# Kernel tuning notes

Hardware: AMD Instinct MI355X
Metric: run time of the kernel (lower is better)

## Reference

```python
import jax, jax.numpy as jnp
import numpy as np

D = 1024  # model_dim; d_ff == model_dim in this module
EPS = 1e-6

def setup_inputs() -> dict:
    key = jax.random.key(0)
    ks = jax.random.split(key, 8)
    s = 1.0 / np.sqrt(D)
    sg = 1.0 / np.sqrt(2 * D)
    return {
        "x": jax.random.normal(ks[0], (8, 2048, D), dtype=jnp.float32),
        "w1": jax.random.uniform(ks[1], (D, D), jnp.float32, -s, s),
        "b1": jnp.zeros((D,), jnp.float32),
        "w2": jax.random.uniform(ks[2], (D, D), jnp.float32, -s, s),
        "b2": jnp.zeros((D,), jnp.float32),
        "ln_g": jnp.ones((D,), jnp.float32),
        "ln_b": jnp.zeros((D,), jnp.float32),
        "wg": jax.random.uniform(ks[3], (2 * D, 2 * D), jnp.float32, -sg, sg),
        "bg": jnp.zeros((2 * D,), jnp.float32),
    }

def _layernorm(x, g, b):
    mu = jnp.mean(x, axis=-1, keepdims=True)
    var = jnp.mean(jnp.square(x - mu), axis=-1, keepdims=True)
    return (x - mu) * jax.lax.rsqrt(var + EPS) * g + b

def reference(x, w1, b1, w2, b2, ln_g, ln_b, wg, bg):
    B, S, d = x.shape
    # cumulative average: tril-normalized mask matmul == prefix-sum / position
    denom = jnp.arange(1, S + 1, dtype=x.dtype)[:, None]  # [S,1]
    avg = jnp.cumsum(x, axis=1) / denom                    # [B,S,D]
    # PositionwiseFeedForward (dropout is identity at inference)
    inter = jax.nn.relu(_layernorm(avg, ln_g, ln_b) @ w1 + b1)
    avg_out = inter @ w2 + b2 + avg
    # gating
    gates = jnp.concatenate([x, avg_out], axis=-1) @ wg + bg  # [B,S,2D]
    in_g, fg_g = jnp.split(gates, 2, axis=-1)
    gated = jax.nn.sigmoid(in_g) * x + jax.nn.sigmoid(fg_g) * avg_out
    return gated, avg_out
```

## Files before the change

### kernel.cpp

```cpp
#include <hip/hip_runtime.h>

typedef unsigned short u16;
typedef __attribute__((ext_vector_type(8))) short short8;
typedef __attribute__((ext_vector_type(8))) unsigned short ushort8;
typedef __attribute__((ext_vector_type(4))) float f32x4;
typedef __attribute__((ext_vector_type(4))) unsigned short u16x4;

#define DEV static __device__ __forceinline__

DEV u16 f2bf(float f){
    unsigned u = __float_as_uint(f);
    u += 0x7fffu + ((u >> 16) & 1u);
    return (u16)(u >> 16);
}
DEV float bf2f(u16 h){ return __uint_as_float(((unsigned)h) << 16); }
DEV float sigm(float v){ return 1.f / (1.f + __expf(-v)); }

DEV f32x4 MF(short8 a, short8 b, f32x4 c){
    return __builtin_amdgcn_mfma_f32_16x16x32_bf16(a, b, c, 0, 0, 0);
}
DEV void gload16(const void* g, u16* l){
    __builtin_amdgcn_global_load_lds(
        (const __attribute__((address_space(1))) void*)g,
        (__attribute__((address_space(3))) void*)l, 16, 0, 0);
}
DEV void stage_half(const char* gp, size_t K2, u16* dst){
    gload16(gp, dst);
    gload16(gp + (K2 << 3), dst + 512);
}

#define SBAR()   asm volatile("s_barrier" ::: "memory")
#define WVM(n)   asm volatile("s_waitcnt vmcnt(" #n ")" ::: "memory")
#define WLG(n)   asm volatile("s_waitcnt lgkmcnt(" #n ")" ::: "memory")
#define SCB()    __builtin_amdgcn_sched_barrier(0)

constexpr int Bn = 8, Sn = 2048, Dn = 1024;
constexpr int CH = 128, NC = Sn / CH;
constexpr size_t NTOK = (size_t)Bn * Sn;

__global__ __launch_bounds__(256) void k_wcvt(const float* __restrict__ w,
                                              u16* __restrict__ wt,
                                              int Kd, int Nd)
{
    __shared__ float tile[32][33];
    int nbn = Nd / 32;
    int bk = blockIdx.x / nbn, bn = blockIdx.x % nbn;
    int lx = threadIdx.x & 31, ly = threadIdx.x >> 5;
    #pragma unroll
    for (int i = 0; i < 32; i += 8)
        tile[ly + i][lx] = w[(size_t)(bk * 32 + ly + i) * Nd + bn * 32 + lx];
    __syncthreads();
    #pragma unroll
    for (int i = 0; i < 32; i += 8)
        wt[(size_t)(bn * 32 + ly + i) * Kd + bk * 32 + lx] = f2bf(tile[lx][ly + i]);
}

__global__ __launch_bounds__(256) void k_psum(const float* __restrict__ x,
                                              float* __restrict__ part)
{
    int bx = blockIdx.x;
    int dblk = bx & 3; bx >>= 2;
    int c = bx & (NC - 1), b = bx >> 4;
    int d = dblk * 256 + threadIdx.x;
    const float* px = x + ((size_t)b * Sn + (size_t)c * CH) * Dn + d;
    float s = 0.f;
    #pragma unroll 4
    for (int i = 0; i < CH; i++) s += px[(size_t)i * Dn];
    part[((size_t)b * NC + c) * Dn + d] = s;
}

__global__ __launch_bounds__(256) void k_pscan(float* part)
{
    int g = blockIdx.x * 256 + threadIdx.x;
    int b = g >> 10, d = g & 1023;
    float run = 0.f;
    #pragma unroll
    for (int c = 0; c < NC; c++){
        size_t idx = ((size_t)b * NC + c) * Dn + d;
        float v = part[idx]; part[idx] = run; run += v;
    }
}

__global__ __launch_bounds__(256) void k_avg(const float* __restrict__ x,
                                             const float* __restrict__ part,
                                             u16* __restrict__ avg,
                                             u16* __restrict__ cat)
{
    int bx = blockIdx.x;
    int dblk = bx & 3; bx >>= 2;
    int c = bx & (NC - 1), b = bx >> 4;
    int d = dblk * 256 + threadIdx.x;
    const float* px = x   + ((size_t)b * Sn + (size_t)c * CH) * Dn + d;
    u16*         pa = avg + ((size_t)b * Sn + (size_t)c * CH) * Dn + d;
    u16*         pc = cat + ((size_t)b * Sn + (size_t)c * CH) * 2048 + d;
    float run = part[((size_t)b * NC + c) * Dn + d];
    for (int i = 0; i < CH; i++){
        float v = px[(size_t)i * Dn];
        run += v;
        int s = c * CH + i;
        pa[(size_t)i * Dn] = f2bf(run / (float)(s + 1));
        pc[(size_t)i * 2048] = f2bf(v);
    }
}

__global__ __launch_bounds__(256) void k_ln(const u16* __restrict__ avg,
                                            const float* __restrict__ g,
                                            const float* __restrict__ bta,
                                            u16* __restrict__ out)
{
    size_t row = blockIdx.x;
    int t = threadIdx.x;
    u16x4 hv = ((const u16x4*)(avg + row * Dn))[t];
    float4 v = { bf2f(hv[0]), bf2f(hv[1]), bf2f(hv[2]), bf2f(hv[3]) };
    float s = v.x + v.y + v.z + v.w;
    float q = v.x * v.x + v.y * v.y + v.z * v.z + v.w * v.w;
    #pragma unroll
    for (int o = 32; o > 0; o >>= 1){
        s += __shfl_down(s, o, 64);
        q += __shfl_down(q, o, 64);
    }
    __shared__ float rs[4], rq[4];
    __shared__ float smu, srstd;
    int wid = t >> 6, lane = t & 63;
    if (lane == 0){ rs[wid] = s; rq[wid] = q; }
    __syncthreads();
    if (t == 0){
        float S = rs[0] + rs[1] + rs[2] + rs[3];
        float Q = rq[0] + rq[1] + rq[2] + rq[3];
        float mu = S * (1.f / Dn);
        float var = Q * (1.f / Dn) - mu * mu;
        smu = mu; srstd = rsqrtf(var + 1e-6f);
    }
    __syncthreads();
    float mu = smu, rstd = srstd;
    int d0 = t * 4;
    float4 gg = ((const float4*)g)[t];
    float4 bb = ((const float4*)bta)[t];
    u16x4 o;
    o[0] = f2bf((v.x - mu) * rstd * gg.x + bb.x);
    o[1] = f2bf((v.y - mu) * rstd * gg.y + bb.y);
    o[2] = f2bf((v.z - mu) * rstd * gg.z + bb.z);
    o[3] = f2bf((v.w - mu) * rstd * gg.w + bb.w);
    *(u16x4*)(out + row * Dn + d0) = o;
}

template<int EPI>
__global__ __launch_bounds__(512, 2)
void k_gemm(const u16* __restrict__ A, const u16* __restrict__ Bt,
            const float* __restrict__ bias,
            float* __restrict__ of, u16* __restrict__ ob,
            const u16* __restrict__ resid,
            int M, int N, int K)
{
    __shared__ u16 smem[2][2][2][8192];

    int nbn = (EPI == 3) ? 8 : (N >> 8);
    int nwg = (M >> 8) * nbn;
    int bid = blockIdx.x;
    int swz = (bid & 7) * (nwg >> 3) + (bid >> 3);
    int bm = swz / nbn, bn = swz - bm * nbn;
    int m0 = bm << 8;
    int n0 = (EPI == 3) ? (bn << 7) : (bn << 8);

    int tid  = threadIdx.x;
    int wid  = tid >> 6, lane = tid & 63;
    int wm   = wid >> 2, wn = wid & 3;
    int fr   = lane & 15, q = lane >> 4;

    int srow = (wid << 4) + (lane >> 3);
    int cb   = ((lane & 7) << 4) ^ (((lane >> 3) & 7) << 4);
    size_t K2 = (size_t)K * 2;
    int b1base = (EPI == 3) ? (1024 + n0) : (n0 + 128);
    const char* gA0 = (const char*)A  + (size_t)(m0 + srow) * K2 + cb;
    const char* gA1 = (const char*)A  + (size_t)(m0 + 128 + srow) * K2 + cb;
    const char* gB0 = (const char*)Bt + (size_t)(n0 + srow) * K2 + cb;
    const char* gB1 = (const char*)Bt + (size_t)(b1base + srow) * K2 + cb;
    int w16 = wid << 10;

    int xorE = (lane & 7) << 3;
    int cbE0 = ((q << 3) ^ xorE);
    int cbE1 = cbE0 ^ 32;
    int aOff = (wm * 64 + fr) * 64;
    int bOff = (wn * 32 + fr) * 64;

    f32x4 acc[8][4] = {};
    short8 a0f[4][2], a1f[4][2], b0f[2][2], b1f[2][2];
    int NT = K >> 6;

#define ST_A0(t) stage_half(gA0 + (size_t)(t) * 128, K2, &smem[(t)&1][0][0][w16])
#define ST_A1(t) stage_half(gA1 + (size_t)(t) * 128, K2, &smem[(t)&1][0][1][w16])
#define ST_B0(t) stage_half(gB0 + (size_t)(t) * 128, K2, &smem[(t)&1][1][0][w16])
#define ST_B1(t) stage_half(gB1 + (size_t)(t) * 128, K2, &smem[(t)&1][1][1][w16])
#define RD_A(Fr, t, half) { const u16* _p = &smem[(t)&1][0][half][0];           \
    _Pragma("unroll") for (int i = 0; i < 4; i++){                              \
        Fr[i][0] = *(const short8*)&_p[aOff + i * 1024 + cbE0];                 \
        Fr[i][1] = *(const short8*)&_p[aOff + i * 1024 + cbE1]; } }
#define RD_B(Fr, t, half) { const u16* _p = &smem[(t)&1][1][half][0];           \
    _Pragma("unroll") for (int i = 0; i < 2; i++){                              \
        Fr[i][0] = *(const short8*)&_p[bOff + i * 1024 + cbE0];                 \
        Fr[i][1] = *(const short8*)&_p[bOff + i * 1024 + cbE1]; } }
#define MMQ(Af, Bf, mo, no)                                                     \
    __builtin_amdgcn_s_setprio(1);                                              \
    _Pragma("unroll") for (int k = 0; k < 2; k++)                               \
        _Pragma("unroll") for (int mi = 0; mi < 4; mi++)                        \
            _Pragma("unroll") for (int ni = 0; ni < 2; ni++)                    \
                acc[mi+(mo)][ni+(no)] = MF(Af[mi][k], Bf[ni][k],                \
                                           acc[mi+(mo)][ni+(no)]);              \
    __builtin_amdgcn_s_setprio(0);

    ST_A0(0); ST_B0(0); ST_A1(0); ST_B1(0);

    for (int t = 0; t + 1 < NT; ++t){
        WVM(4); SBAR();
        ST_A0(t + 1);
        RD_A(a0f, t, 0);
        RD_B(b0f, t, 0);
        WLG(0); SCB();
        MMQ(a0f, b0f, 0, 0);
        WVM(4); SBAR();
        ST_B0(t + 1);
        RD_A(a1f, t, 1);
        WLG(0); SCB();
        MMQ(a1f, b0f, 4, 0);
        WVM(4); SBAR();
        ST_A1(t + 1);
        RD_B(b1f, t, 1);
        WLG(0); SCB();
        MMQ(a1f, b1f, 4, 2);
        ST_B1(t + 1);
        MMQ(a0f, b1f, 0, 2);
    }
    {
        int t = NT - 1;
        WVM(4); SBAR();
        RD_A(a0f, t, 0);
        RD_B(b0f, t, 0);
        WLG(0); SCB();
        MMQ(a0f, b0f, 0, 0);
        WVM(2); SBAR();
        RD_A(a1f, t, 1);
        WLG(0); SCB();
        MMQ(a1f, b0f, 4, 0);
        WVM(0); SBAR();
        RD_B(b1f, t, 1);
        WLG(0); SCB();
        MMQ(a1f, b1f, 4, 2);
        MMQ(a0f, b1f, 0, 2);
    }

    int col = lane & 15, rb = q * 4;

    if constexpr (EPI == 3){
        u16* s_in = &smem[0][0][0][0];
        u16* s_fg = s_in + 32768;
        float bi[2], bf_[2];
        #pragma unroll
        for (int ni = 0; ni < 2; ni++){
            bi[ni]  = bias[n0 + wn * 32 + ni * 16 + col];
            bf_[ni] = bias[1024 + n0 + wn * 32 + ni * 16 + col];
        }
        SBAR();
        #pragma unroll
        for (int mi = 0; mi < 8; mi++){
            int lrow = ((mi & 4) << 5) + wm * 64 + ((mi & 3) << 4) + rb;
            #pragma unroll
            for (int ni = 0; ni < 2; ni++){
                int c  = wn * 32 + ni * 16 + col;
                int cp = c ^ (q << 4);
                #pragma unroll
                for (int r = 0; r < 4; r++){
                    int row = lrow + r;
                    s_in[row * 128 + cp] = f2bf(sigm(acc[mi][ni][r] + bi[ni]));
                    s_fg[row * 128 + cp] = f2bf(sigm(acc[mi][ni + 2][r] + bf_[ni]));
                }
            }
        }
        WLG(0); SBAR();
        int rbase = wid * 32;
        #pragma unroll
        for (int rg = 0; rg < 8; rg++){
            int b4  = rbase + rg * 4;
            int row = b4 + (lane >> 4);
            int sw  = ((b4 >> 2) & 3) << 4;
            int c0  = (lane & 15) * 8;
            int cp  = c0 ^ sw;
            ushort8 iv = *(const ushort8*)&s_in[row * 128 + cp];
            ushort8 fv = *(const ushort8*)&s_fg[row * 128 + cp];
            size_t ga = (size_t)(m0 + row) * 2048 + n0 + c0;
            ushort8 xv = *(const ushort8*)&A[ga];
            ushort8 av = *(const ushort8*)&A[ga + 1024];
            size_t gb = (size_t)(m0 + row) * Dn + n0 + c0;
            float4 o0, o1;
            o0.x = bf2f(iv[0]) * bf2f(xv[0]) + bf2f(fv[0]) * bf2f(av[0]);
            o0.y = bf2f(iv[1]) * bf2f(xv[1]) + bf2f(fv[1]) * bf2f(av[1]);
            o0.z = bf2f(iv[2]) * bf2f(xv[2]) + bf2f(fv[2]) * bf2f(av[2]);
            o0.w = bf2f(iv[3]) * bf2f(xv[3]) + bf2f(fv[3]) * bf2f(av[3]);
            o1.x = bf2f(iv[4]) * bf2f(xv[4]) + bf2f(fv[4]) * bf2f(av[4]);
            o1.y = bf2f(iv[5]) * bf2f(xv[5]) + bf2f(fv[5]) * bf2f(av[5]);
            o1.z = bf2f(iv[6]) * bf2f(xv[6]) + bf2f(fv[6]) * bf2f(av[6]);
            o1.w = bf2f(iv[7]) * bf2f(xv[7]) + bf2f(fv[7]) * bf2f(av[7]);
            *(float4*)&of[gb] = o0;
            *(float4*)&of[gb + 4] = o1;
        }
        return;
    }

    #pragma unroll
    for (int mi = 0; mi < 8; mi++){
        int lrow = m0 + ((mi & 4) << 5) + wm * 64 + ((mi & 3) << 4) + rb;
        #pragma unroll
        for (int ni = 0; ni < 4; ni++){
            int gn = n0 + ((ni & 2) << 6) + wn * 32 + ((ni & 1) << 4) + col;
            float bv = bias[gn];
            #pragma unroll
            for (int r = 0; r < 4; r++){
                int gm = lrow + r;
                float v = acc[mi][ni][r] + bv;
                if constexpr (EPI == 1){
                    ob[(size_t)gm * N + gn] = f2bf(fmaxf(v, 0.f));
                } else {
                    v += bf2f(resid[(size_t)gm * N + gn]);
                    of[(size_t)gm * N + gn] = v;
                    ob[(size_t)gm * 2 * N + N + gn] = f2bf(v);
                }
            }
        }
    }
}

extern "C" void kernel_launch(void* const* d_in, const int* in_sizes, int n_in,
                              void* d_out, int out_size, void* d_ws, size_t ws_size,
                              hipStream_t stream)
{
    const float* x   = (const float*)d_in[0];
    const float* w1  = (const float*)d_in[1];
    const float* b1  = (const float*)d_in[2];
    const float* w2  = (const float*)d_in[3];
    const float* b2  = (const float*)d_in[4];
    const float* lng = (const float*)d_in[5];
    const float* lnb = (const float*)d_in[6];
    const float* wg  = (const float*)d_in[7];
    const float* bg  = (const float*)d_in[8];

    float* gated   = (float*)d_out;
    float* avg_out = (float*)d_out + NTOK * Dn;

    char* ws = (char*)d_ws;
    u16*   w1t   = (u16*)  (ws + (0ull   << 20));
    u16*   w2t   = (u16*)  (ws + (2ull   << 20));
    u16*   wgt   = (u16*)  (ws + (4ull   << 20));
    float* part  = (float*)(ws + (12ull  << 20));
    u16*   avg   = (u16*)  (ws + (16ull  << 20));
    u16*   ln    = (u16*)  (ws + (80ull  << 20));
    u16*   inter = (u16*)  (ws + (112ull << 20));
    u16*   cat   = (u16*)  (ws + (144ull << 20));

    k_wcvt<<<dim3(32 * 32), 256, 0, stream>>>(w1, w1t, Dn, Dn);
    k_wcvt<<<dim3(32 * 32), 256, 0, stream>>>(w2, w2t, Dn, Dn);
    k_wcvt<<<dim3(64 * 64), 256, 0, stream>>>(wg, wgt, 2 * Dn, 2 * Dn);

    k_psum <<<dim3(Bn * NC * 4), 256, 0, stream>>>(x, part);
    k_pscan<<<dim3(Bn * Dn / 256), 256, 0, stream>>>(part);
    k_avg  <<<dim3(Bn * NC * 4), 256, 0, stream>>>(x, part, avg, cat);

    k_ln<<<dim3((int)NTOK), 256, 0, stream>>>(avg, lng, lnb, ln);

    k_gemm<1><<<dim3((int)(NTOK / 256) * (Dn / 256)), 512, 0, stream>>>(
        ln, w1t, b1, nullptr, inter, nullptr, (int)NTOK, Dn, Dn);
    k_gemm<2><<<dim3((int)(NTOK / 256) * (Dn / 256)), 512, 0, stream>>>(
        inter, w2t, b2, avg_out, cat, avg, (int)NTOK, Dn, Dn);

    k_gemm<3><<<dim3((int)(NTOK / 256) * 8), 512, 0, stream>>>(
        cat, wgt, bg, gated, nullptr, nullptr, (int)NTOK, 2 * Dn, 2 * Dn);
}
```

Measured before the change: 304.0 us.

## Rewrite GEMM main loop with BK=32 single-stage pipeline and templated M-tile

Replaces the quarter-staged 256x256, BK=64 GEMM loop with a simpler double-buffered loop that uses BK=32 and stages whole A/B tiles each iteration. The M-tile is now a template parameter: the first two GEMMs use 128-row tiles, doubling the grid, and the gate GEMM keeps 256 rows. The gate epilogue is reorganised so each warp covers input and forget halves in separate columns and writes through LDS in two passes. Intent is to raise occupancy and parallelism and simplify scheduling. The cost is more barriers per unit of K and the loss of the fine-grained load/compute interleave.

```diff
diff --git a/kernel.cpp b/kernel.cpp
--- a/kernel.cpp
+++ b/kernel.cpp
@@ -23,10 +23,6 @@
     __builtin_amdgcn_global_load_lds(
         (const __attribute__((address_space(1))) void*)g,
         (__attribute__((address_space(3))) void*)l, 16, 0, 0);
-}
-DEV void stage_half(const char* gp, size_t K2, u16* dst){
-    gload16(gp, dst);
-    gload16(gp + (K2 << 3), dst + 512);
 }
 
 #define SBAR()   asm volatile("s_barrier" ::: "memory")
@@ -144,7 +140,7 @@
     *(u16x4*)(out + row * Dn + d0) = o;
 }
 
-template<int EPI>
+template<int EPI, int BM>
 __global__ __launch_bounds__(512, 2)
 void k_gemm(const u16* __restrict__ A, const u16* __restrict__ Bt,
             const float* __restrict__ bias,
@@ -152,14 +148,17 @@
             const u16* __restrict__ resid,
             int M, int N, int K)
 {
-    __shared__ u16 smem[2][2][2][8192];
+    constexpr int MFR  = BM / 32;
+    constexpr int AL   = BM / 128;
+    constexpr int HALF = (BM + 256) * 32;
+    __shared__ u16 smem[2 * HALF];
 
     int nbn = (EPI == 3) ? 8 : (N >> 8);
-    int nwg = (M >> 8) * nbn;
+    int nwg = (M / BM) * nbn;
     int bid = blockIdx.x;
     int swz = (bid & 7) * (nwg >> 3) + (bid >> 3);
     int bm = swz / nbn, bn = swz - bm * nbn;
-    int m0 = bm << 8;
+    int m0 = bm * BM;
     int n0 = (EPI == 3) ? (bn << 7) : (bn << 8);
 
     int tid  = threadIdx.x;
@@ -167,155 +166,139 @@
     int wm   = wid >> 2, wn = wid & 3;
     int fr   = lane & 15, q = lane >> 4;
 
-    int srow = (wid << 4) + (lane >> 3);
-    int cb   = ((lane & 7) << 4) ^ (((lane >> 3) & 7) << 4);
+    int l4 = (lane & 3) << 4;
+    int lr = lane >> 2;
     size_t K2 = (size_t)K * 2;
-    int b1base = (EPI == 3) ? (1024 + n0) : (n0 + 128);
-    const char* gA0 = (const char*)A  + (size_t)(m0 + srow) * K2 + cb;
-    const char* gA1 = (const char*)A  + (size_t)(m0 + 128 + srow) * K2 + cb;
-    const char* gB0 = (const char*)Bt + (size_t)(n0 + srow) * K2 + cb;
-    const char* gB1 = (const char*)Bt + (size_t)(b1base + srow) * K2 + cb;
-    int w16 = wid << 10;
-
-    int xorE = (lane & 7) << 3;
-    int cbE0 = ((q << 3) ^ xorE);
-    int cbE1 = cbE0 ^ 32;
-    int aOff = (wm * 64 + fr) * 64;
-    int bOff = (wn * 32 + fr) * 64;
-
-    f32x4 acc[8][4] = {};
-    short8 a0f[4][2], a1f[4][2], b0f[2][2], b1f[2][2];
-    int NT = K >> 6;
-
-#define ST_A0(t) stage_half(gA0 + (size_t)(t) * 128, K2, &smem[(t)&1][0][0][w16])
-#define ST_A1(t) stage_half(gA1 + (size_t)(t) * 128, K2, &smem[(t)&1][0][1][w16])
-#define ST_B0(t) stage_half(gB0 + (size_t)(t) * 128, K2, &smem[(t)&1][1][0][w16])
-#define ST_B1(t) stage_half(gB1 + (size_t)(t) * 128, K2, &smem[(t)&1][1][1][w16])
-#define RD_A(Fr, t, half) { const u16* _p = &smem[(t)&1][0][half][0];           \
-    _Pragma("unroll") for (int i = 0; i < 4; i++){                              \
-        Fr[i][0] = *(const short8*)&_p[aOff + i * 1024 + cbE0];                 \
-        Fr[i][1] = *(const short8*)&_p[aOff + i * 1024 + cbE1]; } }
-#define RD_B(Fr, t, half) { const u16* _p = &smem[(t)&1][1][half][0];           \
-    _Pragma("unroll") for (int i = 0; i < 2; i++){                              \
-        Fr[i][0] = *(const short8*)&_p[bOff + i * 1024 + cbE0];                 \
-        Fr[i][1] = *(const short8*)&_p[bOff + i * 1024 + cbE1]; } }
-#define MMQ(Af, Bf, mo, no)                                                     \
-    __builtin_amdgcn_s_setprio(1);                                              \
-    _Pragma("unroll") for (int k = 0; k < 2; k++)                               \
-        _Pragma("unroll") for (int mi = 0; mi < 4; mi++)                        \
-            _Pragma("unroll") for (int ni = 0; ni < 2; ni++)                    \
-                acc[mi+(mo)][ni+(no)] = MF(Af[mi][k], Bf[ni][k],                \
-                                           acc[mi+(mo)][ni+(no)]);              \
-    __builtin_amdgcn_s_setprio(0);
-
-    ST_A0(0); ST_B0(0); ST_A1(0); ST_B1(0);
-
-    for (int t = 0; t + 1 < NT; ++t){
-        WVM(4); SBAR();
-        ST_A0(t + 1);
-        RD_A(a0f, t, 0);
-        RD_B(b0f, t, 0);
+    const char* gA = (const char*)A + (size_t)(m0 + wid * (BM / 8) + lr) * K2 + l4;
+    int brow = n0 + wid * 32 + lr;
+    if (EPI == 3 && wid >= 4) brow += 896;
+    const char* gB = (const char*)Bt + (size_t)brow * K2 + l4;
+    int aDst = (wid * (BM / 8)) * 32;
+    int bDst = BM * 32 + (wid * 32) * 32;
+
+    int aOff = (wm * (BM / 2) + fr) * 32 + (q << 3);
+    int bOff = BM * 32 + (wn * 64 + fr) * 32 + (q << 3);
+
+    f32x4 acc[MFR][4] = {};
+    short8 af[MFR], bf[4];
+    int NT = K >> 5;
+
+#define STAGE(t) {                                                          \
+    u16* _bp = smem + (((t) & 1) ? HALF : 0);                               \
+    _Pragma("unroll")                                                       \
+    for (int j = 0; j < AL; j++)                                            \
+        gload16(gA + (size_t)(t) * 64 + (size_t)j * 16 * K2,                \
+                _bp + aDst + j * 512);                                      \
+    _Pragma("unroll")                                                       \
+    for (int j = 0; j < 2; j++)                                             \
+        gload16(gB + (size_t)(t) * 64 + (size_t)j * 16 * K2,                \
+                _bp + bDst + j * 512);                                      \
+}
+
+    STAGE(0);
+    for (int t = 0; t < NT; ++t){
+        WVM(0); SBAR();
+        if (t + 1 < NT) STAGE(t + 1);
+        const u16* cp = smem + ((t & 1) ? HALF : 0);
+        #pragma unroll
+        for (int ni = 0; ni < 4; ni++)
+            bf[ni] = *(const short8*)&cp[bOff + ni * 512];
+        #pragma unroll
+        for (int mi = 0; mi < 4; mi++)
+            af[mi] = *(const short8*)&cp[aOff + mi * 512];
         WLG(0); SCB();
-        MMQ(a0f, b0f, 0, 0);
-        WVM(4); SBAR();
-        ST_B0(t + 1);
-        RD_A(a1f, t, 1);
-        WLG(0); SCB();
-        MMQ(a1f, b0f, 4, 0);
-        WVM(4); SBAR();
-        ST_A1(t + 1);
-        RD_B(b1f, t, 1);
-        WLG(0); SCB();
-        MMQ(a1f, b1f, 4, 2);
-        ST_B1(t + 1);
-        MMQ(a0f, b1f, 0, 2);
-    }
-    {
-        int t = NT - 1;
-        WVM(4); SBAR();
-        RD_A(a0f, t, 0);
-        RD_B(b0f, t, 0);
-        WLG(0); SCB();
-        MMQ(a0f, b0f, 0, 0);
-        WVM(2); SBAR();
-        RD_A(a1f, t, 1);
-        WLG(0); SCB();
-        MMQ(a1f, b0f, 4, 0);
-        WVM(0); SBAR();
-        RD_B(b1f, t, 1);
-        WLG(0); SCB();
-        MMQ(a1f, b1f, 4, 2);
-        MMQ(a0f, b1f, 0, 2);
+        __builtin_amdgcn_s_setprio(1);
+        #pragma unroll
+        for (int mi = 0; mi < 4; mi++)
+            #pragma unroll
+            for (int ni = 0; ni < 4; ni++)
+                acc[mi][ni] = MF(af[mi], bf[ni], acc[mi][ni]);
+        __builtin_amdgcn_s_setprio(0);
+        if constexpr (MFR == 8){
+            #pragma unroll
+            for (int mi = 0; mi < 4; mi++)
+                af[mi + 4] = *(const short8*)&cp[aOff + (mi + 4) * 512];
+            WLG(0); SCB();
+            __builtin_amdgcn_s_setprio(1);
+            #pragma unroll
+            for (int mi = 0; mi < 4; mi++)
+                #pragma unroll
+                for (int ni = 0; ni < 4; ni++)
+                    acc[mi + 4][ni] = MF(af[mi + 4], bf[ni], acc[mi + 4][ni]);
+            __builtin_amdgcn_s_setprio(0);
+        }
     }
 
     int col = lane & 15, rb = q * 4;
 
     if constexpr (EPI == 3){
-        u16* s_in = &smem[0][0][0][0];
-        u16* s_fg = s_in + 32768;
-        float bi[2], bf_[2];
-        #pragma unroll
-        for (int ni = 0; ni < 2; ni++){
-            bi[ni]  = bias[n0 + wn * 32 + ni * 16 + col];
-            bf_[ni] = bias[1024 + n0 + wn * 32 + ni * 16 + col];
+        u16* s_in = smem;
+        u16* s_fg = smem + 16384;
+        float bv[4];
+        #pragma unroll
+        for (int ni = 0; ni < 4; ni++){
+            int c = (wn & 1) * 64 + ni * 16 + col;
+            bv[ni] = bias[((wn < 2) ? n0 : 1024 + n0) + c];
         }
-        SBAR();
-        #pragma unroll
-        for (int mi = 0; mi < 8; mi++){
-            int lrow = ((mi & 4) << 5) + wm * 64 + ((mi & 3) << 4) + rb;
-            #pragma unroll
-            for (int ni = 0; ni < 2; ni++){
-                int c  = wn * 32 + ni * 16 + col;
-                int cp = c ^ (q << 4);
+        #pragma unroll
+        for (int p = 0; p < 2; p++){
+            SBAR();
+            if (wm == p){
                 #pragma unroll
-                for (int r = 0; r < 4; r++){
-                    int row = lrow + r;
-                    s_in[row * 128 + cp] = f2bf(sigm(acc[mi][ni][r] + bi[ni]));
-                    s_fg[row * 128 + cp] = f2bf(sigm(acc[mi][ni + 2][r] + bf_[ni]));
+                for (int mi = 0; mi < 8; mi++){
+                    #pragma unroll
+                    for (int ni = 0; ni < 4; ni++){
+                        int c  = (wn & 1) * 64 + ni * 16 + col;
+                        u16* dst = (wn < 2) ? s_in : s_fg;
+                        #pragma unroll
+                        for (int r = 0; r < 4; r++){
+                            int row = mi * 16 + rb + r;
+                            int cpx = c ^ (((row >> 2) & 3) << 4);
+                            dst[row * 128 + cpx] =
+                                f2bf(sigm(acc[mi][ni][r] + bv[ni]));
+                        }
+                    }
                 }
             }
-        }
-        WLG(0); SBAR();
-        int rbase = wid * 32;
-        #pragma unroll
-        for (int rg = 0; rg < 8; rg++){
-            int b4  = rbase + rg * 4;
-            int row = b4 + (lane >> 4);
-            int sw  = ((b4 >> 2) & 3) << 4;
-            int c0  = (lane & 15) * 8;
-            int cp  = c0 ^ sw;
-            ushort8 iv = *(const ushort8*)&s_in[row * 128 + cp];
-            ushort8 fv = *(const ushort8*)&s_fg[row * 128 + cp];
-            size_t ga = (size_t)(m0 + row) * 2048 + n0 + c0;
-            ushort8 xv = *(const ushort8*)&A[ga];
-            ushort8 av = *(const ushort8*)&A[ga + 1024];
-            size_t gb = (size_t)(m0 + row) * Dn + n0 + c0;
-            float4 o0, o1;
-            o0.x = bf2f(iv[0]) * bf2f(xv[0]) + bf2f(fv[0]) * bf2f(av[0]);
-            o0.y = bf2f(iv[1]) * bf2f(xv[1]) + bf2f(fv[1]) * bf2f(av[1]);
-            o0.z = bf2f(iv[2]) * bf2f(xv[2]) + bf2f(fv[2]) * bf2f(av[2]);
-            o0.w = bf2f(iv[3]) * bf2f(xv[3]) + bf2f(fv[3]) * bf2f(av[3]);
-            o1.x = bf2f(iv[4]) * bf2f(xv[4]) + bf2f(fv[4]) * bf2f(av[4]);
-            o1.y = bf2f(iv[5]) * bf2f(xv[5]) + bf2f(fv[5]) * bf2f(av[5]);
-            o1.z = bf2f(iv[6]) * bf2f(xv[6]) + bf2f(fv[6]) * bf2f(av[6]);
-            o1.w = bf2f(iv[7]) * bf2f(xv[7]) + bf2f(fv[7]) * bf2f(av[7]);
-            *(float4*)&of[gb] = o0;
-            *(float4*)&of[gb + 4] = o1;
+            WLG(0); SBAR();
+            #pragma unroll
+            for (int rg = 0; rg < 4; rg++){
+                int row_l = wid * 16 + rg * 4 + q;
+                int grow  = m0 + p * 128 + row_l;
+                int c0 = fr * 8;
+                int cpx = c0 ^ (((row_l >> 2) & 3) << 4);
+                ushort8 iv = *(const ushort8*)&s_in[row_l * 128 + cpx];
+                ushort8 fv = *(const ushort8*)&s_fg[row_l * 128 + cpx];
+                size_t ga = (size_t)grow * 2048 + n0 + c0;
+                ushort8 xv = *(const ushort8*)&A[ga];
+                ushort8 av = *(const ushort8*)&A[ga + 1024];
+                size_t gb = (size_t)grow * Dn + n0 + c0;
+                float4 o0, o1;
+                o0.x = bf2f(iv[0]) * bf2f(xv[0]) + bf2f(fv[0]) * bf2f(av[0]);
+                o0.y = bf2f(iv[1]) * bf2f(xv[1]) + bf2f(fv[1]) * bf2f(av[1]);
+                o0.z = bf2f(iv[2]) * bf2f(xv[2]) + bf2f(fv[2]) * bf2f(av[2]);
+                o0.w = bf2f(iv[3]) * bf2f(xv[3]) + bf2f(fv[3]) * bf2f(av[3]);
+                o1.x = bf2f(iv[4]) * bf2f(xv[4]) + bf2f(fv[4]) * bf2f(av[4]);
+                o1.y = bf2f(iv[5]) * bf2f(xv[5]) + bf2f(fv[5]) * bf2f(av[5]);
+                o1.z = bf2f(iv[6]) * bf2f(xv[6]) + bf2f(fv[6]) * bf2f(av[6]);
+                o1.w = bf2f(iv[7]) * bf2f(xv[7]) + bf2f(fv[7]) * bf2f(av[7]);
+                *(float4*)&of[gb] = o0;
+                *(float4*)&of[gb + 4] = o1;
+            }
         }
         return;
     }
 
     #pragma unroll
-    for (int mi = 0; mi < 8; mi++){
-        int lrow = m0 + ((mi & 4) << 5) + wm * 64 + ((mi & 3) << 4) + rb;
+    for (int mi = 0; mi < MFR; mi++){
         #pragma unroll
         for (int ni = 0; ni < 4; ni++){
-            int gn = n0 + ((ni & 2) << 6) + wn * 32 + ((ni & 1) << 4) + col;
-            float bv = bias[gn];
+            int gn = n0 + wn * 64 + ni * 16 + col;
+            float bvv = bias[gn];
             #pragma unroll
             for (int r = 0; r < 4; r++){
-                int gm = lrow + r;
-                float v = acc[mi][ni][r] + bv;
+                int gm = m0 + wm * (BM / 2) + mi * 16 + rb + r;
+                float v = acc[mi][ni][r] + bvv;
                 if constexpr (EPI == 1){
                     ob[(size_t)gm * N + gn] = f2bf(fmaxf(v, 0.f));
                 } else {
@@ -365,11 +348,11 @@
 
     k_ln<<<dim3((int)NTOK), 256, 0, stream>>>(avg, lng, lnb, ln);
 
-    k_gemm<1><<<dim3((int)(NTOK / 256) * (Dn / 256)), 512, 0, stream>>>(
+    k_gemm<1, 128><<<dim3((int)(NTOK / 128) * (Dn / 256)), 512, 0, stream>>>(
         ln, w1t, b1, nullptr, inter, nullptr, (int)NTOK, Dn, Dn);
-    k_gemm<2><<<dim3((int)(NTOK / 256) * (Dn / 256)), 512, 0, stream>>>(
+    k_gemm<2, 128><<<dim3((int)(NTOK / 128) * (Dn / 256)), 512, 0, stream>>>(
         inter, w2t, b2, avg_out, cat, avg, (int)NTOK, Dn, Dn);
 
-    k_gemm<3><<<dim3((int)(NTOK / 256) * 8), 512, 0, stream>>>(
+    k_gemm<3, 256><<<dim3((int)(NTOK / 256) * 8), 512, 0, stream>>>(
         cat, wgt, bg, gated, nullptr, nullptr, (int)NTOK, 2 * Dn, 2 * Dn);
 }
```

Result: slower. 343.8 us (+13.1%).

## Fuse cumulative average and layernorm into one row-sequential kernel

Applied to the files above, without the earlier changes.

Merges the running-average kernel and the layernorm kernel so each block walks a chunk of rows, computing the prefix average in fp32 and immediately normalizing it. This removes the bf16 re-read of avg and a launch. The chunk size is halved to keep more blocks in the prefix-sum stages. The fused kernel has only one block per chunk and a block barrier per row, which limits memory-level parallelism.

```diff
diff --git a/kernel.cpp b/kernel.cpp
--- a/kernel.cpp
+++ b/kernel.cpp
@@ -35,7 +35,7 @@
 #define SCB()    __builtin_amdgcn_sched_barrier(0)
 
 constexpr int Bn = 8, Sn = 2048, Dn = 1024;
-constexpr int CH = 128, NC = Sn / CH;
+constexpr int CH = 64, NC = Sn / CH;
 constexpr size_t NTOK = (size_t)Bn * Sn;
 
 __global__ __launch_bounds__(256) void k_wcvt(const float* __restrict__ w,
@@ -60,7 +60,7 @@
 {
     int bx = blockIdx.x;
     int dblk = bx & 3; bx >>= 2;
-    int c = bx & (NC - 1), b = bx >> 4;
+    int c = bx & (NC - 1), b = bx >> 5;
     int d = dblk * 256 + threadIdx.x;
     const float* px = x + ((size_t)b * Sn + (size_t)c * CH) * Dn + d;
     float s = 0.f;
@@ -81,67 +81,64 @@
     }
 }
 
-__global__ __launch_bounds__(256) void k_avg(const float* __restrict__ x,
-                                             const float* __restrict__ part,
-                                             u16* __restrict__ avg,
-                                             u16* __restrict__ cat)
-{
-    int bx = blockIdx.x;
-    int dblk = bx & 3; bx >>= 2;
-    int c = bx & (NC - 1), b = bx >> 4;
-    int d = dblk * 256 + threadIdx.x;
-    const float* px = x   + ((size_t)b * Sn + (size_t)c * CH) * Dn + d;
-    u16*         pa = avg + ((size_t)b * Sn + (size_t)c * CH) * Dn + d;
-    u16*         pc = cat + ((size_t)b * Sn + (size_t)c * CH) * 2048 + d;
-    float run = part[((size_t)b * NC + c) * Dn + d];
-    for (int i = 0; i < CH; i++){
-        float v = px[(size_t)i * Dn];
-        run += v;
-        int s = c * CH + i;
-        pa[(size_t)i * Dn] = f2bf(run / (float)(s + 1));
-        pc[(size_t)i * 2048] = f2bf(v);
-    }
-}
-
-__global__ __launch_bounds__(256) void k_ln(const u16* __restrict__ avg,
-                                            const float* __restrict__ g,
-                                            const float* __restrict__ bta,
-                                            u16* __restrict__ out)
-{
-    size_t row = blockIdx.x;
+__global__ __launch_bounds__(256) void k_avgln(const float* __restrict__ x,
+                                               const float* __restrict__ part,
+                                               const float* __restrict__ g,
+                                               const float* __restrict__ bta,
+                                               u16* __restrict__ avg,
+                                               u16* __restrict__ cat,
+                                               u16* __restrict__ ln)
+{
+    int blk = blockIdx.x;
+    int c = blk & (NC - 1), b = blk >> 5;
     int t = threadIdx.x;
-    u16x4 hv = ((const u16x4*)(avg + row * Dn))[t];
-    float4 v = { bf2f(hv[0]), bf2f(hv[1]), bf2f(hv[2]), bf2f(hv[3]) };
-    float s = v.x + v.y + v.z + v.w;
-    float q = v.x * v.x + v.y * v.y + v.z * v.z + v.w * v.w;
-    #pragma unroll
-    for (int o = 32; o > 0; o >>= 1){
-        s += __shfl_down(s, o, 64);
-        q += __shfl_down(q, o, 64);
-    }
-    __shared__ float rs[4], rq[4];
-    __shared__ float smu, srstd;
     int wid = t >> 6, lane = t & 63;
-    if (lane == 0){ rs[wid] = s; rq[wid] = q; }
-    __syncthreads();
-    if (t == 0){
-        float S = rs[0] + rs[1] + rs[2] + rs[3];
-        float Q = rq[0] + rq[1] + rq[2] + rq[3];
-        float mu = S * (1.f / Dn);
-        float var = Q * (1.f / Dn) - mu * mu;
-        smu = mu; srstd = rsqrtf(var + 1e-6f);
-    }
-    __syncthreads();
-    float mu = smu, rstd = srstd;
     int d0 = t * 4;
+    size_t rowbase = (size_t)b * Sn + (size_t)c * CH;
+
+    const float4* px = (const float4*)(x + rowbase * Dn + d0);
+    u16* pa = avg + rowbase * Dn + d0;
+    u16* pc = cat + rowbase * 2048 + d0;
+    u16* pl = ln  + rowbase * Dn + d0;
+
+    float4 run = ((const float4*)(part + ((size_t)b * NC + c) * Dn + d0))[0];
     float4 gg = ((const float4*)g)[t];
     float4 bb = ((const float4*)bta)[t];
-    u16x4 o;
-    o[0] = f2bf((v.x - mu) * rstd * gg.x + bb.x);
-    o[1] = f2bf((v.y - mu) * rstd * gg.y + bb.y);
-    o[2] = f2bf((v.z - mu) * rstd * gg.z + bb.z);
-    o[3] = f2bf((v.w - mu) * rstd * gg.w + bb.w);
-    *(u16x4*)(out + row * Dn + d0) = o;
+
+    __shared__ float rs[2][4], rq[2][4];
+
+    for (int i = 0; i < CH; i++){
+        float4 v = px[(size_t)i * (Dn / 4)];
+        run.x += v.x; run.y += v.y; run.z += v.z; run.w += v.w;
+        int s = c * CH + i;
+        float inv = 1.f / (float)(s + 1);
+        float4 a = { run.x * inv, run.y * inv, run.z * inv, run.w * inv };
+
+        float s4 = a.x + a.y + a.z + a.w;
+        float q4 = a.x * a.x + a.y * a.y + a.z * a.z + a.w * a.w;
+        #pragma unroll
+        for (int o = 32; o > 0; o >>= 1){
+            s4 += __shfl_down(s4, o, 64);
+            q4 += __shfl_down(q4, o, 64);
+        }
+        int par = i & 1;
+        if (lane == 0){ rs[par][wid] = s4; rq[par][wid] = q4; }
+        __syncthreads();
+        float mu = (rs[par][0] + rs[par][1] + rs[par][2] + rs[par][3]) * (1.f / Dn);
+        float Q  = (rq[par][0] + rq[par][1] + rq[par][2] + rq[par][3]) * (1.f / Dn);
+        float rstd = rsqrtf(Q - mu * mu + 1e-6f);
+
+        u16x4 oa = { f2bf(a.x), f2bf(a.y), f2bf(a.z), f2bf(a.w) };
+        u16x4 ox = { f2bf(v.x), f2bf(v.y), f2bf(v.z), f2bf(v.w) };
+        u16x4 ol;
+        ol[0] = f2bf((a.x - mu) * rstd * gg.x + bb.x);
+        ol[1] = f2bf((a.y - mu) * rstd * gg.y + bb.y);
+        ol[2] = f2bf((a.z - mu) * rstd * gg.z + bb.z);
+        ol[3] = f2bf((a.w - mu) * rstd * gg.w + bb.w);
+        *(u16x4*)(pa + (size_t)i * Dn)   = oa;
+        *(u16x4*)(pc + (size_t)i * 2048) = ox;
+        *(u16x4*)(pl + (size_t)i * Dn)   = ol;
+    }
 }
 
 template<int EPI>
@@ -361,9 +358,7 @@
 
     k_psum <<<dim3(Bn * NC * 4), 256, 0, stream>>>(x, part);
     k_pscan<<<dim3(Bn * Dn / 256), 256, 0, stream>>>(part);
-    k_avg  <<<dim3(Bn * NC * 4), 256, 0, stream>>>(x, part, avg, cat);
-
-    k_ln<<<dim3((int)NTOK), 256, 0, stream>>>(avg, lng, lnb, ln);
+    k_avgln<<<dim3(Bn * NC), 256, 0, stream>>>(x, part, lng, lnb, avg, cat, ln);
 
     k_gemm<1><<<dim3((int)(NTOK / 256) * (Dn / 256)), 512, 0, stream>>>(
         ln, w1t, b1, nullptr, inter, nullptr, (int)NTOK, Dn, Dn);
```

New measurement: 311.2 us. 2.4% more time.
